# Kernel tuning notes

Measured on AMD Instinct MI355X. Metric: run time of the kernel, lower is better.

The kernel has to match this reference:

```python
import jax, jax.numpy as jnp
import numpy as np

B, C, N, T = 64, 16, 4096, 12   # batch, channels, num_nodes, timesteps
APT = 10                        # adaptive-embedding size
NUM_SUPPORTS = 3                # 2 fixed + 1 adaptive
ORDER = 2                       # diffusion hops


def _rand_adj(k):
    # random row-stochastic transition matrix (stand-in for normalized graph support)
    a = jax.random.uniform(k, (N, N), jnp.float32)
    return a / jnp.sum(a, axis=1, keepdims=True)


def setup_inputs() -> dict:
    key = jax.random.key(0)
    ks = jax.random.split(key, 7)
    x = jax.random.normal(ks[0], (B, C, N, T), jnp.float32)
    support0 = _rand_adj(ks[1])
    support1 = _rand_adj(ks[2])
    nodevec1 = jax.random.normal(ks[3], (N, APT), jnp.float32)
    nodevec2 = jax.random.normal(ks[4], (APT, N), jnp.float32)
    c_cat = C * (NUM_SUPPORTS * ORDER + 1)  # 7*C
    W = jax.random.normal(ks[5], (C, c_cat), jnp.float32) * 0.05  # 1x1 conv weight
    b = jnp.zeros((C,), jnp.float32)
    return dict(x=x, support0=support0, support1=support1,
                nodevec1=nodevec1, nodevec2=nodevec2, W=W, b=b)


def _nconv(x, a):
    # torch: einsum('ncvl,vw->ncwl')
    return jnp.einsum('bcnt,nm->bcmt', x, a)


def reference(x, support0, support1, nodevec1, nodevec2, W, b):
    # adaptive adjacency: softmax(relu(E1 @ E2), dim=1)
    adp = jax.nn.softmax(jax.nn.relu(nodevec1 @ nodevec2), axis=1)
    supports = [support0, support1, adp]
    outs = [x]
    for a in supports:  # small fixed loop over supports/hops
        x1 = _nconv(x, a)
        outs.append(x1)
        x2 = _nconv(x1, a)
        outs.append(x2)
    h = jnp.concatenate(outs, axis=1)            # [B, 7C, N, T]
    h = jnp.einsum('bknt,ck->bcnt', h, W) + b[None, :, None, None]  # 1x1 conv
    # dropout omitted (eval mode / deterministic reference)
    return x + h                                  # residual add
```

## Files before the change

kernel.cpp:

```cpp
#include <hip/hip_runtime.h>
#include <hip/hip_bf16.h>

#define B_  64
#define C_  16
#define N_  4096
#define T_  12
#define ROWS_ (B_ * T_ * C_)
#define NT_ 64

typedef __attribute__((ext_vector_type(4))) float f32x4;
typedef __attribute__((ext_vector_type(8))) short s16x8;
typedef __attribute__((ext_vector_type(4))) short s16x4;
typedef __attribute__((ext_vector_type(8))) int   i32x8;
typedef __attribute__((ext_vector_type(4))) int   i32x4;

__device__ __forceinline__ ushort f2bf(float f) {
    unsigned u = __builtin_bit_cast(unsigned, f);
    u += 0x7fffu + ((u >> 16) & 1u);
    return (ushort)(u >> 16);
}

__device__ __forceinline__ uchar f2fp8(float f) {
    float a = fabsf(f);
    unsigned s = (__builtin_bit_cast(unsigned, f) >> 24) & 0x80u;
    if (a >= 448.f) return (uchar)(s | 0x7E);
    if (a < 0.015625f) {
        int m = (int)rintf(a * 512.f);
        return (uchar)(s | (unsigned)m);
    }
    unsigned u = __builtin_bit_cast(unsigned, a);
    unsigned r = (u + 0x7FFFFu + ((u >> 20) & 1u)) >> 20;
    return (uchar)(s | (r - 960u));
}

__device__ __forceinline__ f32x4 mfma16x16x16bf16(s16x4 a, s16x4 b, f32x4 c) {
#if __has_builtin(__builtin_amdgcn_mfma_f32_16x16x16_bf16)
    return __builtin_amdgcn_mfma_f32_16x16x16_bf16(a, b, c, 0, 0, 0);
#elif __has_builtin(__builtin_amdgcn_mfma_f32_16x16x16bf16_1k)
    return __builtin_amdgcn_mfma_f32_16x16x16bf16_1k(a, b, c, 0, 0, 0);
#else
    f32x4 d = c;
    asm volatile("v_mfma_f32_16x16x16_bf16 %0, %1, %2, %0"
                 : "+v"(d) : "v"(a), "v"(b));
    return d;
#endif
}

typedef const __attribute__((address_space(1))) unsigned int* gas_t;
typedef __attribute__((address_space(3))) unsigned int* las_t;
__device__ __forceinline__ void gload16(const ushort* g, ushort* l) {
    __builtin_amdgcn_global_load_lds((gas_t)(const void*)g, (las_t)(void*)l, 16, 0, 0);
}
__device__ __forceinline__ void gload16b(const uchar* g, uchar* l) {
    __builtin_amdgcn_global_load_lds((gas_t)(const void*)g, (las_t)(void*)l, 16, 0, 0);
}

__global__ __launch_bounds__(256)
void pack_x(const float* __restrict__ x, const float* __restrict__ W,
            const float* __restrict__ bias, ushort* __restrict__ X2,
            uchar* __restrict__ X8, float* __restrict__ racc) {
    __shared__ float xs[16][32][13];
    __shared__ float sW[16][16];
    __shared__ float sb[16];
    const int t  = threadIdx.x;
    const int n0 = blockIdx.x * 32;
    const int b  = blockIdx.y;
    sW[t >> 4][t & 15] = W[(t >> 4) * 112 + (t & 15)];
    if (t < 16) sb[t] = bias[t];
    #pragma unroll
    for (int p0 = 0; p0 < 2; ++p0) {
        int p = p0 * 256 + t;
        int c = p >> 5, nn = p & 31;
        const float* src = x + (size_t)((b * 16 + c) * 4096 + n0 + nn) * 12;
        float tmp[12];
        *(float4*)(tmp)     = *(const float4*)(src);
        *(float4*)(tmp + 4) = *(const float4*)(src + 4);
        *(float4*)(tmp + 8) = *(const float4*)(src + 8);
        #pragma unroll
        for (int k = 0; k < 12; ++k) xs[c][nn][k] = tmp[k];
    }
    __syncthreads();
    #pragma unroll
    for (int i = 0; i < 24; ++i) {
        int e = i * 256 + t;
        int nn = e & 31, rowi = e >> 5;
        int tt = rowi >> 4, c = rowi & 15;
        float xv = xs[c][nn][tt];
        float acc = xv + sb[c];
        #pragma unroll
        for (int cp = 0; cp < 16; ++cp) acc += sW[c][cp] * xs[cp][nn][tt];
        size_t row = (size_t)(b * 12 + tt) * 16 + c;
        racc[row * 4096 + n0 + nn] = acc;
        X2[row * 4096 + n0 + nn]   = f2bf(xv);
        X8[row * 4096 + n0 + nn]   = f2fp8(xv);
    }
}

__global__ __launch_bounds__(256)
void transpose_fp8(const float* __restrict__ S, uchar* __restrict__ D, float scale) {
    __shared__ float ld[64][65];
    const int t  = threadIdx.x;
    const int m0 = blockIdx.x * 64;
    const int n0 = blockIdx.y * 64;
    #pragma unroll
    for (int it = 0; it < 4; ++it) {
        int row = it * 16 + (t >> 4);
        int col = (t & 15) * 4;
        float4 v = *(const float4*)&S[(size_t)(n0 + row) * 4096 + m0 + col];
        ld[row][col] = v.x; ld[row][col + 1] = v.y;
        ld[row][col + 2] = v.z; ld[row][col + 3] = v.w;
    }
    __syncthreads();
    #pragma unroll
    for (int it = 0; it < 8; ++it) {
        int mr = it * 8 + (t >> 5);
        int nc = (t & 31) * 2;
        ushort p = (ushort)f2fp8(ld[nc][mr] * scale) |
                   ((ushort)f2fp8(ld[nc + 1][mr] * scale) << 8);
        *(ushort*)&D[(size_t)(m0 + mr) * 4096 + n0 + nc] = p;
    }
}

__global__ __launch_bounds__(256)
void adp_rows(const float* __restrict__ e1, const float* __restrict__ e2,
              float* __restrict__ V, float* __restrict__ maxn, float* __restrict__ sumn) {
    const int n = blockIdx.x, t = threadIdx.x;
    __shared__ float se1[10];
    __shared__ float red[8];
    if (t < 10) se1[t] = e1[n * 10 + t];
    __syncthreads();
    float v[16];
    float mx = -1e30f;
    #pragma unroll
    for (int i = 0; i < 16; ++i) {
        int m = i * 256 + t;
        float s = 0.f;
        #pragma unroll
        for (int k = 0; k < 10; ++k) s += se1[k] * e2[k * 4096 + m];
        s = fmaxf(s, 0.f);
        v[i] = s;
        mx = fmaxf(mx, s);
        V[(size_t)n * 4096 + m] = s;
    }
    for (int o = 32; o; o >>= 1) mx = fmaxf(mx, __shfl_down(mx, o));
    if ((t & 63) == 0) red[t >> 6] = mx;
    __syncthreads();
    if (t == 0) red[4] = fmaxf(fmaxf(red[0], red[1]), fmaxf(red[2], red[3]));
    __syncthreads();
    mx = red[4];
    float sm = 0.f;
    #pragma unroll
    for (int i = 0; i < 16; ++i) sm += __expf(v[i] - mx);
    for (int o = 32; o; o >>= 1) sm += __shfl_down(sm, o);
    __syncthreads();
    if ((t & 63) == 0) red[t >> 6] = sm;
    __syncthreads();
    if (t == 0) { maxn[n] = mx; sumn[n] = red[0] + red[1] + red[2] + red[3]; }
}

__global__ __launch_bounds__(256)
void adp_norm(const float* __restrict__ V, const float* __restrict__ maxn,
              const float* __restrict__ sumn, ushort* __restrict__ D) {
    __shared__ float ld[64][65];
    const int t  = threadIdx.x;
    const int m0 = blockIdx.x * 64;
    const int n0 = blockIdx.y * 64;
    #pragma unroll
    for (int it = 0; it < 4; ++it) {
        int row = it * 16 + (t >> 4);
        int col = (t & 15) * 4;
        float4 v = *(const float4*)&V[(size_t)(n0 + row) * 4096 + m0 + col];
        ld[row][col] = v.x; ld[row][col + 1] = v.y;
        ld[row][col + 2] = v.z; ld[row][col + 3] = v.w;
    }
    __syncthreads();
    #pragma unroll
    for (int it = 0; it < 8; ++it) {
        int mr = it * 8 + (t >> 5);
        int nc = (t & 31) * 2;
        float va = __expf(ld[nc][mr]     - maxn[n0 + nc])     / sumn[n0 + nc];
        float vb = __expf(ld[nc + 1][mr] - maxn[n0 + nc + 1]) / sumn[n0 + nc + 1];
        unsigned pack = (unsigned)f2bf(va) | ((unsigned)f2bf(vb) << 16);
        *(unsigned*)&D[(size_t)(m0 + mr) * 4096 + n0 + nc] = pack;
    }
}

__global__ __launch_bounds__(512, 2)
void gemm_mix(const ushort* __restrict__ Xp, const ushort* __restrict__ Bt,
              ushort* __restrict__ Yp, float* __restrict__ racc,
              const float* __restrict__ W, int cblk, int writeY) {
    __shared__ ushort lds[65536];
    const int tid  = threadIdx.x;
    const int lane = tid & 63;
    const int wid  = tid >> 6;
    const int wm   = wid >> 2;
    const int wn   = wid & 3;
    const int lr   = lane & 15;
    const int lq   = lane >> 4;
    const int fsw  = (lane & 7) << 3;

    int flat = blockIdx.y * gridDim.x + blockIdx.x;
    int swz  = (flat & 7) * 96 + (flat >> 3);
    const size_t r0 = (size_t)(swz >> 4) * 256;
    const size_t c0 = (size_t)(swz & 15) * 256;

#define AIDX(b, mi, ks) (((b) * 32768)          + (((((mi) * 32 + wm * 16 + lr) * 64) + (ks) * 32 + lq * 8) ^ fsw))
#define BIDX(b, nj, ks) (((b) * 32768 + 16384)  + ((((wn * 64 + (nj) * 16 + lr) * 64) + (ks) * 32 + lq * 8) ^ fsw))

#define STAGE(P, rg0, tt, h, mat)                                                      \
    {                                                                                  \
        ushort* _base = &lds[((tt) & 1) * 32768 + (mat) * 16384 + (h) * 8192];         \
        const size_t _k0 = (size_t)(tt) * 64;                                          \
        _Pragma("unroll")                                                              \
        for (int _i = 0; _i < 2; ++_i) {                                               \
            int _e   = (_i * 512 + tid) * 8;                                           \
            int _row = _e >> 6;                                                        \
            int _col = (_e & 63) ^ ((_row & 7) << 3);                                  \
            gload16(&(P)[((rg0) + (h) * 128 + _row) * 4096 + _k0 + _col], &_base[_e]); \
        }                                                                              \
    }

#define PHASE(MI0, STAGE_STMT)                                                                                 \
    {                                                                                                          \
        STAGE_STMT;                                                                                            \
        s16x8 a0 = *(const s16x8*)&lds[AIDX(b, (MI0),     0)];                                                 \
        s16x8 a1 = *(const s16x8*)&lds[AIDX(b, (MI0),     1)];                                                 \
        s16x8 a2 = *(const s16x8*)&lds[AIDX(b, (MI0) + 1, 0)];                                                 \
        s16x8 a3 = *(const s16x8*)&lds[AIDX(b, (MI0) + 1, 1)];                                                 \
        __builtin_amdgcn_s_barrier();                                                                          \
        __builtin_amdgcn_s_setprio(1);                                                                         \
        _Pragma("unroll")                                                                                      \
        for (int nj = 0; nj < 4; ++nj) {                                                                       \
            acc[(MI0)][nj]     = __builtin_amdgcn_mfma_f32_16x16x32_bf16(a0, bfr[nj][0], acc[(MI0)][nj], 0, 0, 0);     \
            acc[(MI0)][nj]     = __builtin_amdgcn_mfma_f32_16x16x32_bf16(a1, bfr[nj][1], acc[(MI0)][nj], 0, 0, 0);     \
            acc[(MI0) + 1][nj] = __builtin_amdgcn_mfma_f32_16x16x32_bf16(a2, bfr[nj][0], acc[(MI0) + 1][nj], 0, 0, 0); \
            acc[(MI0) + 1][nj] = __builtin_amdgcn_mfma_f32_16x16x32_bf16(a3, bfr[nj][1], acc[(MI0) + 1][nj], 0, 0, 0); \
        }                                                                                                      \
        __builtin_amdgcn_s_setprio(0);                                                                         \
    }

    f32x4 acc[8][4] = {};

    STAGE(Xp, r0, 0, 0, 0);
    STAGE(Xp, r0, 0, 1, 0);
    STAGE(Bt, c0, 0, 0, 1);
    STAGE(Bt, c0, 0, 1, 1);
    STAGE(Xp, r0, 1, 0, 0);
    STAGE(Bt, c0, 1, 0, 1);
    asm volatile("s_waitcnt vmcnt(4)" ::: "memory");
    __builtin_amdgcn_s_barrier();

    for (int t = 0; t < NT_; ++t) {
        const int b = t & 1;
        s16x8 bfr[4][2];
        if (t + 1 < NT_) STAGE(Xp, r0, t + 1, 1, 0);
        #pragma unroll
        for (int nj = 0; nj < 4; ++nj) {
            bfr[nj][0] = *(const s16x8*)&lds[BIDX(b, nj, 0)];
            bfr[nj][1] = *(const s16x8*)&lds[BIDX(b, nj, 1)];
        }
        PHASE(0, {});
        __builtin_amdgcn_s_barrier();
        PHASE(2, { if (t + 1 < NT_) STAGE(Bt, c0, t + 1, 1, 1); });
        __builtin_amdgcn_s_barrier();
        PHASE(4, { if (t + 2 < NT_) STAGE(Xp, r0, t + 2, 0, 0); });
        __builtin_amdgcn_s_barrier();
        PHASE(6, { if (t + 2 < NT_) STAGE(Bt, c0, t + 2, 0, 1); });
        if (t < NT_ - 2)       { asm volatile("s_waitcnt vmcnt(4)" ::: "memory"); }
        else if (t == NT_ - 2) { asm volatile("s_waitcnt vmcnt(0)" ::: "memory"); }
        __builtin_amdgcn_sched_barrier(0);
        __builtin_amdgcn_s_barrier();
    }

    if (writeY) {
        #pragma unroll
        for (int mi = 0; mi < 8; ++mi) {
            #pragma unroll
            for (int nj = 0; nj < 4; ++nj) {
                const int col = wn * 64 + nj * 16 + lr;
                #pragma unroll
                for (int r = 0; r < 4; ++r) {
                    const int rr = mi * 32 + wm * 16 + lq * 4 + r;
                    lds[(rr * 256 + col) ^ ((rr & 7) << 3)] = f2bf(acc[mi][nj][r]);
                }
            }
        }
        __syncthreads();
        #pragma unroll
        for (int it = 0; it < 16; ++it) {
            int e = it * 4096 + tid * 8;
            int row = e >> 8, colu = e & 255;
            s16x8 v = *(const s16x8*)&lds[e ^ ((row & 7) << 3)];
            *(s16x8*)&Yp[(r0 + row) * 4096 + c0 + colu] = v;
        }
    }

    {
        const float4 wv4 = *(const float4*)&W[(size_t)lr * 112 + cblk + lq * 4];
        s16x4 wf;
        wf[0] = (short)f2bf(wv4.x); wf[1] = (short)f2bf(wv4.y);
        wf[2] = (short)f2bf(wv4.z); wf[3] = (short)f2bf(wv4.w);
        #pragma unroll
        for (int mi = 0; mi < 8; ++mi) {
            #pragma unroll
            for (int nj = 0; nj < 4; ++nj) {
                s16x4 cb;
                cb[0] = (short)f2bf(acc[mi][nj][0]); cb[1] = (short)f2bf(acc[mi][nj][1]);
                cb[2] = (short)f2bf(acc[mi][nj][2]); cb[3] = (short)f2bf(acc[mi][nj][3]);
                f32x4 d = mfma16x16x16bf16(wf, cb, (f32x4){0.f, 0.f, 0.f, 0.f});
                const size_t row = r0 + (size_t)mi * 32 + wm * 16 + lq * 4;
                const size_t col = c0 + wn * 64 + nj * 16 + lr;
                #pragma unroll
                for (int r = 0; r < 4; ++r) {
                    float* p = &racc[(row + r) * 4096 + col];
                    *p += d[r];
                }
            }
        }
    }
#undef AIDX
#undef BIDX
#undef STAGE
#undef PHASE
}

__device__ __forceinline__ i32x8 ldfrag8(const uchar* lds8, int rbase, int row, int lq) {
    const int sw = (row & 7) << 4;
    const int b  = rbase + row * 128;
    i32x4 lo = *(const i32x4*)&lds8[b + ((lq * 32) ^ sw)];
    i32x4 hi = *(const i32x4*)&lds8[b + ((lq * 32 + 16) ^ sw)];
    return (i32x8){lo[0], lo[1], lo[2], lo[3], hi[0], hi[1], hi[2], hi[3]};
}

__global__ __launch_bounds__(512, 2)
void gemm_fp8(const uchar* __restrict__ Xp, const uchar* __restrict__ Bt,
              uchar* __restrict__ Yp, float* __restrict__ racc,
              const float* __restrict__ W, int cblk, int writeY,
              int sA, int sB) {
    __shared__ uchar lds8[131072];
    const int tid  = threadIdx.x;
    const int lane = tid & 63;
    const int wid  = tid >> 6;
    const int wm   = wid >> 2;
    const int wn   = wid & 3;
    const int lr   = lane & 15;
    const int lq   = lane >> 4;

    int flat = blockIdx.y * gridDim.x + blockIdx.x;
    int swz  = (flat & 7) * 96 + (flat >> 3);
    const size_t r0 = (size_t)(swz >> 4) * 256;
    const size_t c0 = (size_t)(swz & 15) * 256;

#define STAGE8(P, rg0, tt, h, mat)                                                       \
    {                                                                                    \
        uchar* _base = &lds8[((tt) & 1) * 65536 + (mat) * 32768 + (h) * 16384];          \
        const size_t _k0 = (size_t)(tt) * 128;                                           \
        _Pragma("unroll")                                                                \
        for (int _i = 0; _i < 2; ++_i) {                                                 \
            int _e   = (_i * 512 + tid) * 16;                                            \
            int _row = _e >> 7;                                                          \
            int _col = (_e & 127) ^ ((_row & 7) << 4);                                   \
            gload16b(&(P)[((rg0) + (h) * 128 + _row) * 4096 + _k0 + _col], &_base[_e]);  \
        }                                                                                \
    }

    f32x4 acc[8][4] = {};

    STAGE8(Xp, r0, 0, 0, 0);
    STAGE8(Xp, r0, 0, 1, 0);
    STAGE8(Bt, c0, 0, 0, 1);
    STAGE8(Bt, c0, 0, 1, 1);
    STAGE8(Xp, r0, 1, 0, 0);
    STAGE8(Bt, c0, 1, 0, 1);
    asm volatile("s_waitcnt vmcnt(4)" ::: "memory");
    __builtin_amdgcn_s_barrier();

    for (int t = 0; t < 32; ++t) {
        const int bb = (t & 1) * 65536;
        i32x8 bf[4];
        if (t + 1 < 32) STAGE8(Xp, r0, t + 1, 1, 0);
        #pragma unroll
        for (int nj = 0; nj < 4; ++nj)
            bf[nj] = ldfrag8(lds8, bb + 32768, wn * 64 + nj * 16 + lr, lq);
        i32x8 af0 = ldfrag8(lds8, bb,       wm * 16 + lr, lq);
        i32x8 af1 = ldfrag8(lds8, bb,  32 + wm * 16 + lr, lq);
        i32x8 af2 = ldfrag8(lds8, bb,  64 + wm * 16 + lr, lq);
        i32x8 af3 = ldfrag8(lds8, bb,  96 + wm * 16 + lr, lq);
        if (t + 1 < 32) STAGE8(Bt, c0, t + 1, 1, 1);
        __builtin_amdgcn_s_barrier();
        __builtin_amdgcn_s_setprio(1);
        #pragma unroll
        for (int nj = 0; nj < 4; ++nj) {
            acc[0][nj] = __builtin_amdgcn_mfma_scale_f32_16x16x128_f8f6f4(af0, bf[nj], acc[0][nj], 0, 0, 0, sA, 0, sB);
            acc[1][nj] = __builtin_amdgcn_mfma_scale_f32_16x16x128_f8f6f4(af1, bf[nj], acc[1][nj], 0, 0, 0, sA, 0, sB);
            acc[2][nj] = __builtin_amdgcn_mfma_scale_f32_16x16x128_f8f6f4(af2, bf[nj], acc[2][nj], 0, 0, 0, sA, 0, sB);
            acc[3][nj] = __builtin_amdgcn_mfma_scale_f32_16x16x128_f8f6f4(af3, bf[nj], acc[3][nj], 0, 0, 0, sA, 0, sB);
        }
        __builtin_amdgcn_s_setprio(0);
        __builtin_amdgcn_s_barrier();
        if (t + 2 < 32) STAGE8(Xp, r0, t + 2, 0, 0);
        af0 = ldfrag8(lds8, bb, 128 + wm * 16 + lr, lq);
        af1 = ldfrag8(lds8, bb, 160 + wm * 16 + lr, lq);
        af2 = ldfrag8(lds8, bb, 192 + wm * 16 + lr, lq);
        af3 = ldfrag8(lds8, bb, 224 + wm * 16 + lr, lq);
        if (t + 2 < 32) STAGE8(Bt, c0, t + 2, 0, 1);
        __builtin_amdgcn_s_barrier();
        __builtin_amdgcn_s_setprio(1);
        #pragma unroll
        for (int nj = 0; nj < 4; ++nj) {
            acc[4][nj] = __builtin_amdgcn_mfma_scale_f32_16x16x128_f8f6f4(af0, bf[nj], acc[4][nj], 0, 0, 0, sA, 0, sB);
            acc[5][nj] = __builtin_amdgcn_mfma_scale_f32_16x16x128_f8f6f4(af1, bf[nj], acc[5][nj], 0, 0, 0, sA, 0, sB);
            acc[6][nj] = __builtin_amdgcn_mfma_scale_f32_16x16x128_f8f6f4(af2, bf[nj], acc[6][nj], 0, 0, 0, sA, 0, sB);
            acc[7][nj] = __builtin_amdgcn_mfma_scale_f32_16x16x128_f8f6f4(af3, bf[nj], acc[7][nj], 0, 0, 0, sA, 0, sB);
        }
        __builtin_amdgcn_s_setprio(0);
        if (t < 30)       { asm volatile("s_waitcnt vmcnt(4)" ::: "memory"); }
        else if (t == 30) { asm volatile("s_waitcnt vmcnt(0)" ::: "memory"); }
        __builtin_amdgcn_sched_barrier(0);
        __builtin_amdgcn_s_barrier();
    }

    if (writeY) {
        #pragma unroll
        for (int mi = 0; mi < 8; ++mi) {
            #pragma unroll
            for (int nj = 0; nj < 4; ++nj) {
                const int col = wn * 64 + nj * 16 + lr;
                #pragma unroll
                for (int r = 0; r < 4; ++r) {
                    const int rr = mi * 32 + wm * 16 + lq * 4 + r;
                    lds8[(rr * 256 + col) ^ ((rr & 7) << 4)] = f2fp8(acc[mi][nj][r] * 64.f);
                }
            }
        }
        __syncthreads();
        #pragma unroll
        for (int it = 0; it < 8; ++it) {
            int e = it * 8192 + tid * 16;
            int row = e >> 8, colu = e & 255;
            i32x4 v = *(const i32x4*)&lds8[e ^ ((row & 7) << 4)];
            *(i32x4*)&Yp[(r0 + row) * 4096 + c0 + colu] = v;
        }
    }

    {
        const float4 wv4 = *(const float4*)&W[(size_t)lr * 112 + cblk + lq * 4];
        s16x4 wf;
        wf[0] = (short)f2bf(wv4.x); wf[1] = (short)f2bf(wv4.y);
        wf[2] = (short)f2bf(wv4.z); wf[3] = (short)f2bf(wv4.w);
        #pragma unroll
        for (int mi = 0; mi < 8; ++mi) {
            #pragma unroll
            for (int nj = 0; nj < 4; ++nj) {
                s16x4 cb;
                cb[0] = (short)f2bf(acc[mi][nj][0]); cb[1] = (short)f2bf(acc[mi][nj][1]);
                cb[2] = (short)f2bf(acc[mi][nj][2]); cb[3] = (short)f2bf(acc[mi][nj][3]);
                f32x4 d = mfma16x16x16bf16(wf, cb, (f32x4){0.f, 0.f, 0.f, 0.f});
                const size_t row = r0 + (size_t)mi * 32 + wm * 16 + lq * 4;
                const size_t col = c0 + wn * 64 + nj * 16 + lr;
                #pragma unroll
                for (int r = 0; r < 4; ++r) {
                    float* p = &racc[(row + r) * 4096 + col];
                    *p += d[r];
                }
            }
        }
    }
#undef STAGE8
}

__global__ __launch_bounds__(256)
void final_out(const float* __restrict__ racc, float* __restrict__ out) {
    __shared__ float fr[192][32];
    const int t  = threadIdx.x;
    const int n0 = blockIdx.x * 32;
    const int b  = blockIdx.y;
    #pragma unroll
    for (int i = 0; i < 24; ++i) {
        int e = i * 256 + t;
        int rr = e >> 5, nn = e & 31;
        fr[rr][nn] = racc[((size_t)b * 192 + rr) * 4096 + n0 + nn];
    }
    __syncthreads();
    #pragma unroll
    for (int p0 = 0; p0 < 2; ++p0) {
        int p = p0 * 256 + t;
        int c = p >> 5, nn = p & 31;
        float buf[12];
        #pragma unroll
        for (int tt = 0; tt < 12; ++tt) buf[tt] = fr[tt * 16 + c][nn];
        float* dst = &out[(size_t)((b * 16 + c) * 4096 + n0 + nn) * 12];
        *(float4*)(dst)     = *(float4*)(buf);
        *(float4*)(dst + 4) = *(float4*)(buf + 4);
        *(float4*)(dst + 8) = *(float4*)(buf + 8);
    }
}

extern "C" void kernel_launch(void* const* d_in, const int* in_sizes, int n_in,
                              void* d_out, int out_size, void* d_ws, size_t ws_size,
                              hipStream_t stream) {
    const float* x    = (const float*)d_in[0];
    const float* s0   = (const float*)d_in[1];
    const float* s1   = (const float*)d_in[2];
    const float* e1   = (const float*)d_in[3];
    const float* e2   = (const float*)d_in[4];
    const float* W    = (const float*)d_in[5];
    const float* bias = (const float*)d_in[6];
    float* out = (float*)d_out;

    char* ws = (char*)d_ws;
    const size_t SZ_X2   = (size_t)ROWS_ * 4096 * 2;
    const size_t SZ_RACC = (size_t)ROWS_ * 4096 * 4;
    const size_t SZ_REGA = SZ_X2;
    const size_t SZ_X8   = (size_t)ROWS_ * 4096;
    const size_t SZ_SF   = (size_t)4096 * 4096;

    ushort* X2   = (ushort*)(ws);
    float*  racc = (float*)(ws + SZ_X2);
    char*   REGA = ws + SZ_X2 + SZ_RACC;
    uchar*  X8   = (uchar*)(REGA + SZ_REGA);
    uchar*  SF   = (uchar*)((char*)X8 + SZ_X8);
    ushort* ADT  = (ushort*)((char*)SF + SZ_SF);
    float*  maxn = (float*)((char*)ADT + (size_t)4096 * 4096 * 2);
    float*  sumn = maxn + 4096;

    float*  V     = (float*)REGA;
    uchar*  Y80   = (uchar*)REGA;
    uchar*  Y81   = (uchar*)REGA + SZ_X8;
    ushort* Y1adp = (ushort*)REGA;

    const int S_ONE  = 0x7F7F7F7F;
    const int S_M6   = 0x79797979;
    const int S_M12  = 0x73737373;

    pack_x<<<dim3(128, 64), 256, 0, stream>>>(x, W, bias, X2, X8, racc);
    transpose_fp8<<<dim3(64, 64), 256, 0, stream>>>(s0, SF, 4096.f);
    adp_rows<<<4096, 256, 0, stream>>>(e1, e2, V, maxn, sumn);
    adp_norm<<<dim3(64, 64), 256, 0, stream>>>(V, maxn, sumn, ADT);

    gemm_fp8<<<dim3(16, 48), 512, 0, stream>>>(X8,  SF, Y80, racc, W, 16, 1, S_ONE, S_M12);
    gemm_fp8<<<dim3(16, 48), 512, 0, stream>>>(Y80, SF, Y80, racc, W, 32, 0, S_M6,  S_M12);
    transpose_fp8<<<dim3(64, 64), 256, 0, stream>>>(s1, SF, 4096.f);
    gemm_fp8<<<dim3(16, 48), 512, 0, stream>>>(X8,  SF, Y81, racc, W, 48, 1, S_ONE, S_M12);
    gemm_fp8<<<dim3(16, 48), 512, 0, stream>>>(Y81, SF, Y81, racc, W, 64, 0, S_M6,  S_M12);
    gemm_mix<<<dim3(16, 48), 512, 0, stream>>>(X2,    ADT, Y1adp, racc, W, 80, 1);
    gemm_mix<<<dim3(16, 48), 512, 0, stream>>>(Y1adp, ADT, Y1adp, racc, W, 96, 0);

    final_out<<<dim3(128, 64), 256, 0, stream>>>(racc, out);
}
```

Measured before the change: 2.135 ms.

## Move residual mix into final pass, init racc in first GEMM, recompute adaptive scores

The self-channel mix and bias are now computed in final_out, which rereads x, so pack_x no longer writes the fp32 racc buffer and the first fp8 GEMM stores its result instead of read-modify-writing. The 4096x4096 relu-score matrix V is no longer materialized; adp_make recomputes the rank-10 products from the embeddings before normalizing. This removes several full-size global memory passes in exchange for extra x reads in the final kernel and a small amount of recomputed arithmetic.

```diff
diff --git a/kernel.cpp b/kernel.cpp
--- a/kernel.cpp
+++ b/kernel.cpp
@@ -56,17 +56,12 @@
 }
 
 __global__ __launch_bounds__(256)
-void pack_x(const float* __restrict__ x, const float* __restrict__ W,
-            const float* __restrict__ bias, ushort* __restrict__ X2,
-            uchar* __restrict__ X8, float* __restrict__ racc) {
+void pack_x(const float* __restrict__ x, ushort* __restrict__ X2,
+            uchar* __restrict__ X8) {
     __shared__ float xs[16][32][13];
-    __shared__ float sW[16][16];
-    __shared__ float sb[16];
     const int t  = threadIdx.x;
     const int n0 = blockIdx.x * 32;
     const int b  = blockIdx.y;
-    sW[t >> 4][t & 15] = W[(t >> 4) * 112 + (t & 15)];
-    if (t < 16) sb[t] = bias[t];
     #pragma unroll
     for (int p0 = 0; p0 < 2; ++p0) {
         int p = p0 * 256 + t;
@@ -86,13 +81,9 @@
         int nn = e & 31, rowi = e >> 5;
         int tt = rowi >> 4, c = rowi & 15;
         float xv = xs[c][nn][tt];
-        float acc = xv + sb[c];
-        #pragma unroll
-        for (int cp = 0; cp < 16; ++cp) acc += sW[c][cp] * xs[cp][nn][tt];
         size_t row = (size_t)(b * 12 + tt) * 16 + c;
-        racc[row * 4096 + n0 + nn] = acc;
-        X2[row * 4096 + n0 + nn]   = f2bf(xv);
-        X8[row * 4096 + n0 + nn]   = f2fp8(xv);
+        X2[row * 4096 + n0 + nn] = f2bf(xv);
+        X8[row * 4096 + n0 + nn] = f2fp8(xv);
     }
 }
 
@@ -123,7 +114,7 @@
 
 __global__ __launch_bounds__(256)
 void adp_rows(const float* __restrict__ e1, const float* __restrict__ e2,
-              float* __restrict__ V, float* __restrict__ maxn, float* __restrict__ sumn) {
+              float* __restrict__ maxn, float* __restrict__ sumn) {
     const int n = blockIdx.x, t = threadIdx.x;
     __shared__ float se1[10];
     __shared__ float red[8];
@@ -140,7 +131,6 @@
         s = fmaxf(s, 0.f);
         v[i] = s;
         mx = fmaxf(mx, s);
-        V[(size_t)n * 4096 + m] = s;
     }
     for (int o = 32; o; o >>= 1) mx = fmaxf(mx, __shfl_down(mx, o));
     if ((t & 63) == 0) red[t >> 6] = mx;
@@ -159,27 +149,35 @@
 }
 
 __global__ __launch_bounds__(256)
-void adp_norm(const float* __restrict__ V, const float* __restrict__ maxn,
-              const float* __restrict__ sumn, ushort* __restrict__ D) {
-    __shared__ float ld[64][65];
+void adp_make(const float* __restrict__ e1, const float* __restrict__ e2,
+              const float* __restrict__ maxn, const float* __restrict__ sumn,
+              ushort* __restrict__ D) {
+    __shared__ float se1[64][10];
+    __shared__ float se2[10][64];
     const int t  = threadIdx.x;
     const int m0 = blockIdx.x * 64;
     const int n0 = blockIdx.y * 64;
-    #pragma unroll
-    for (int it = 0; it < 4; ++it) {
-        int row = it * 16 + (t >> 4);
-        int col = (t & 15) * 4;
-        float4 v = *(const float4*)&V[(size_t)(n0 + row) * 4096 + m0 + col];
-        ld[row][col] = v.x; ld[row][col + 1] = v.y;
-        ld[row][col + 2] = v.z; ld[row][col + 3] = v.w;
+    for (int i = t; i < 640; i += 256) ((float*)se1)[i] = e1[n0 * 10 + i];
+    for (int i = t; i < 640; i += 256) {
+        int k = i >> 6, m = i & 63;
+        se2[k][m] = e2[k * 4096 + m0 + m];
     }
     __syncthreads();
     #pragma unroll
     for (int it = 0; it < 8; ++it) {
         int mr = it * 8 + (t >> 5);
         int nc = (t & 31) * 2;
-        float va = __expf(ld[nc][mr]     - maxn[n0 + nc])     / sumn[n0 + nc];
-        float vb = __expf(ld[nc + 1][mr] - maxn[n0 + nc + 1]) / sumn[n0 + nc + 1];
+        float v0 = 0.f, v1 = 0.f;
+        #pragma unroll
+        for (int k = 0; k < 10; ++k) {
+            float e2v = se2[k][mr];
+            v0 += se1[nc][k] * e2v;
+            v1 += se1[nc + 1][k] * e2v;
+        }
+        v0 = fmaxf(v0, 0.f);
+        v1 = fmaxf(v1, 0.f);
+        float va = __expf(v0 - maxn[n0 + nc])     / sumn[n0 + nc];
+        float vb = __expf(v1 - maxn[n0 + nc + 1]) / sumn[n0 + nc + 1];
         unsigned pack = (unsigned)f2bf(va) | ((unsigned)f2bf(vb) << 16);
         *(unsigned*)&D[(size_t)(m0 + mr) * 4096 + n0 + nc] = pack;
     }
@@ -188,7 +186,7 @@
 __global__ __launch_bounds__(512, 2)
 void gemm_mix(const ushort* __restrict__ Xp, const ushort* __restrict__ Bt,
               ushort* __restrict__ Yp, float* __restrict__ racc,
-              const float* __restrict__ W, int cblk, int writeY) {
+              const float* __restrict__ W, int cblk, int writeY, int initR) {
     __shared__ ushort lds[65536];
     const int tid  = threadIdx.x;
     const int lane = tid & 63;
@@ -310,10 +308,15 @@
                 f32x4 d = mfma16x16x16bf16(wf, cb, (f32x4){0.f, 0.f, 0.f, 0.f});
                 const size_t row = r0 + (size_t)mi * 32 + wm * 16 + lq * 4;
                 const size_t col = c0 + wn * 64 + nj * 16 + lr;
-                #pragma unroll
-                for (int r = 0; r < 4; ++r) {
-                    float* p = &racc[(row + r) * 4096 + col];
-                    *p += d[r];
+                if (initR) {
+                    #pragma unroll
+                    for (int r = 0; r < 4; ++r) racc[(row + r) * 4096 + col] = d[r];
+                } else {
+                    #pragma unroll
+                    for (int r = 0; r < 4; ++r) {
+                        float* p = &racc[(row + r) * 4096 + col];
+                        *p += d[r];
+                    }
                 }
             }
         }
@@ -335,8 +338,8 @@
 __global__ __launch_bounds__(512, 2)
 void gemm_fp8(const uchar* __restrict__ Xp, const uchar* __restrict__ Bt,
               uchar* __restrict__ Yp, float* __restrict__ racc,
-              const float* __restrict__ W, int cblk, int writeY,
-              int sA, int sB) {
+              const float* __restrict__ W, int cblk, int writeY, int initR,
+              int sA, int sB, float ysc) {
     __shared__ uchar lds8[131072];
     const int tid  = threadIdx.x;
     const int lane = tid & 63;
@@ -429,7 +432,7 @@
                 #pragma unroll
                 for (int r = 0; r < 4; ++r) {
                     const int rr = mi * 32 + wm * 16 + lq * 4 + r;
-                    lds8[(rr * 256 + col) ^ ((rr & 7) << 4)] = f2fp8(acc[mi][nj][r] * 64.f);
+                    lds8[(rr * 256 + col) ^ ((rr & 7) << 4)] = f2fp8(acc[mi][nj][r] * ysc);
                 }
             }
         }
@@ -458,10 +461,15 @@
                 f32x4 d = mfma16x16x16bf16(wf, cb, (f32x4){0.f, 0.f, 0.f, 0.f});
                 const size_t row = r0 + (size_t)mi * 32 + wm * 16 + lq * 4;
                 const size_t col = c0 + wn * 64 + nj * 16 + lr;
-                #pragma unroll
-                for (int r = 0; r < 4; ++r) {
-                    float* p = &racc[(row + r) * 4096 + col];
-                    *p += d[r];
+                if (initR) {
+                    #pragma unroll
+                    for (int r = 0; r < 4; ++r) racc[(row + r) * 4096 + col] = d[r];
+                } else {
+                    #pragma unroll
+                    for (int r = 0; r < 4; ++r) {
+                        float* p = &racc[(row + r) * 4096 + col];
+                        *p += d[r];
+                    }
                 }
             }
         }
@@ -470,17 +478,36 @@
 }
 
 __global__ __launch_bounds__(256)
-void final_out(const float* __restrict__ racc, float* __restrict__ out) {
+void final_out(const float* __restrict__ racc, const float* __restrict__ x,
+               const float* __restrict__ W, const float* __restrict__ bias,
+               float* __restrict__ out) {
     __shared__ float fr[192][32];
+    __shared__ float xs[16][32][13];
+    __shared__ float sW[16][16];
+    __shared__ float sb[16];
     const int t  = threadIdx.x;
     const int n0 = blockIdx.x * 32;
     const int b  = blockIdx.y;
+    sW[t >> 4][t & 15] = W[(t >> 4) * 112 + (t & 15)];
+    if (t < 16) sb[t] = bias[t];
     #pragma unroll
     for (int i = 0; i < 24; ++i) {
         int e = i * 256 + t;
         int rr = e >> 5, nn = e & 31;
         fr[rr][nn] = racc[((size_t)b * 192 + rr) * 4096 + n0 + nn];
     }
+    #pragma unroll
+    for (int p0 = 0; p0 < 2; ++p0) {
+        int p = p0 * 256 + t;
+        int c = p >> 5, nn = p & 31;
+        const float* src = x + (size_t)((b * 16 + c) * 4096 + n0 + nn) * 12;
+        float tmp[12];
+        *(float4*)(tmp)     = *(const float4*)(src);
+        *(float4*)(tmp + 4) = *(const float4*)(src + 4);
+        *(float4*)(tmp + 8) = *(const float4*)(src + 8);
+        #pragma unroll
+        for (int k = 0; k < 12; ++k) xs[c][nn][k] = tmp[k];
+    }
     __syncthreads();
     #pragma unroll
     for (int p0 = 0; p0 < 2; ++p0) {
@@ -488,7 +515,12 @@
         int c = p >> 5, nn = p & 31;
         float buf[12];
         #pragma unroll
-        for (int tt = 0; tt < 12; ++tt) buf[tt] = fr[tt * 16 + c][nn];
+        for (int tt = 0; tt < 12; ++tt) {
+            float acc = xs[c][nn][tt] + sb[c] + fr[tt * 16 + c][nn];
+            #pragma unroll
+            for (int cp = 0; cp < 16; ++cp) acc += sW[c][cp] * xs[cp][nn][tt];
+            buf[tt] = acc;
+        }
         float* dst = &out[(size_t)((b * 16 + c) * 4096 + n0 + nn) * 12];
         *(float4*)(dst)     = *(float4*)(buf);
         *(float4*)(dst + 4) = *(float4*)(buf + 4);
@@ -524,27 +556,26 @@
     float*  maxn = (float*)((char*)ADT + (size_t)4096 * 4096 * 2);
     float*  sumn = maxn + 4096;
 
-    float*  V     = (float*)REGA;
     uchar*  Y80   = (uchar*)REGA;
     uchar*  Y81   = (uchar*)REGA + SZ_X8;
     ushort* Y1adp = (ushort*)REGA;
 
-    const int S_ONE  = 0x7F7F7F7F;
-    const int S_M6   = 0x79797979;
-    const int S_M12  = 0x73737373;
-
-    pack_x<<<dim3(128, 64), 256, 0, stream>>>(x, W, bias, X2, X8, racc);
+    const int S_ONE = 0x7F7F7F7F;
+    const int S_M6  = 0x79797979;
+    const int S_M12 = 0x73737373;
+
+    pack_x<<<dim3(128, 64), 256, 0, stream>>>(x, X2, X8);
     transpose_fp8<<<dim3(64, 64), 256, 0, stream>>>(s0, SF, 4096.f);
-    adp_rows<<<4096, 256, 0, stream>>>(e1, e2, V, maxn, sumn);
-    adp_norm<<<dim3(64, 64), 256, 0, stream>>>(V, maxn, sumn, ADT);
-
-    gemm_fp8<<<dim3(16, 48), 512, 0, stream>>>(X8,  SF, Y80, racc, W, 16, 1, S_ONE, S_M12);
-    gemm_fp8<<<dim3(16, 48), 512, 0, stream>>>(Y80, SF, Y80, racc, W, 32, 0, S_M6,  S_M12);
+    adp_rows<<<4096, 256, 0, stream>>>(e1, e2, maxn, sumn);
+    adp_make<<<dim3(64, 64), 256, 0, stream>>>(e1, e2, maxn, sumn, ADT);
+
+    gemm_fp8<<<dim3(16, 48), 512, 0, stream>>>(X8,  SF, Y80, racc, W, 16, 1, 1, S_ONE, S_M12, 64.f);
+    gemm_fp8<<<dim3(16, 48), 512, 0, stream>>>(Y80, SF, Y80, racc, W, 32, 0, 0, S_M6,  S_M12, 0.f);
     transpose_fp8<<<dim3(64, 64), 256, 0, stream>>>(s1, SF, 4096.f);
-    gemm_fp8<<<dim3(16, 48), 512, 0, stream>>>(X8,  SF, Y81, racc, W, 48, 1, S_ONE, S_M12);
-    gemm_fp8<<<dim3(16, 48), 512, 0, stream>>>(Y81, SF, Y81, racc, W, 64, 0, S_M6,  S_M12);
-    gemm_mix<<<dim3(16, 48), 512, 0, stream>>>(X2,    ADT, Y1adp, racc, W, 80, 1);
-    gemm_mix<<<dim3(16, 48), 512, 0, stream>>>(Y1adp, ADT, Y1adp, racc, W, 96, 0);
-
-    final_out<<<dim3(128, 64), 256, 0, stream>>>(racc, out);
-}
+    gemm_fp8<<<dim3(16, 48), 512, 0, stream>>>(X8,  SF, Y81, racc, W, 48, 1, 0, S_ONE, S_M12, 64.f);
+    gemm_fp8<<<dim3(16, 48), 512, 0, stream>>>(Y81, SF, Y81, racc, W, 64, 0, 0, S_M6,  S_M12, 0.f);
+    gemm_mix<<<dim3(16, 48), 512, 0, stream>>>(X2,    ADT, Y1adp, racc, W, 80, 1, 0);
+    gemm_mix<<<dim3(16, 48), 512, 0, stream>>>(Y1adp, ADT, Y1adp, racc, W, 96, 0, 0);
+
+    final_out<<<dim3(128, 64), 256, 0, stream>>>(racc, x, W, bias, out);
+}
```

Result: slower. 2.213 ms (+3.6%).
